# Kernel tuning notes

Measured on AMD Instinct MI355X. Metric: run time of the kernel, lower is better.

The kernel has to match this reference:

```python
import jax, jax.numpy as jnp
import numpy as np

N, E, F_IN, F_OUT, E_DIM = 8192, 65536, 256, 64, 32


def _xavier(k, shape, gain):
    fan_out, fan_in = shape
    bound = gain * jnp.sqrt(6.0 / (fan_in + fan_out))
    return jax.random.uniform(k, shape, jnp.float32, -bound, bound)


def setup_inputs() -> dict:
    key = jax.random.key(0)
    ks = jax.random.split(key, 10)
    gain = float(np.sqrt(2.0))  # calculate_gain('relu')
    return {
        "h_neigh": jax.random.normal(ks[0], (N, F_IN), jnp.float32),
        "h_self": jax.random.normal(ks[1], (N, F_IN), jnp.float32),
        "edge_features": jax.random.normal(ks[2], (E, E_DIM), jnp.float32),
        "W_preagg": _xavier(ks[3], (F_OUT, F_IN), gain),
        "W_self": _xavier(ks[4], (F_OUT, F_OUT), gain),
        "W_neigh": _xavier(ks[5], (F_OUT, F_OUT), gain),
        "W_edge": _xavier(ks[6], (F_OUT * F_OUT, E_DIM), gain),
        "b_edge": jnp.zeros((F_OUT * F_OUT,), jnp.float32),
        "src": jax.random.randint(ks[7], (E,), 0, N, jnp.int32),
        "dst": jax.random.randint(ks[8], (E,), 0, N, jnp.int32),
    }


def reference(h_neigh, h_self, edge_features, W_preagg, W_self, W_neigh, W_edge, b_edge, src, dst):
    relu = jax.nn.relu
    # fc_preagg (Linear no-bias + ReLU); dropout p=0 -> identity (eval mode)
    hn = relu(h_neigh @ W_preagg.T)   # [N, F_OUT]
    hs = relu(h_self @ W_preagg.T)    # [N, F_OUT]
    # edge_fc: Linear(edge_dim, F*F) + ReLU, viewed as [E, F, F]
    ew = relu(edge_features @ W_edge.T + b_edge).reshape(E, F_OUT, F_OUT)
    # DGL u_mul_e broadcast: m[e,i,j] = hn[src[e], j] * ew[e,i,j]
    # then mean over in-edges per dst node, then sum over dim i.
    # mean/sum commute with the i-sum, so fold i first: s[e,j] = sum_i ew[e,i,j]
    s = ew.sum(axis=1)                # [E, F_OUT]
    msg = hn[src] * s                 # [E, F_OUT]
    agg = jax.ops.segment_sum(msg, dst, num_segments=N)                      # [N, F_OUT]
    deg = jax.ops.segment_sum(jnp.ones((E,), jnp.float32), dst, num_segments=N)
    neigh = agg / jnp.maximum(deg, 1.0)[:, None]  # mean (0 for isolated nodes, as DGL)
    # fc_self / fc_neigh each include a ReLU, plus the outer ReLU
    z = relu(relu(hs @ W_self.T) + relu(neigh @ W_neigh.T))
    return z
```

## Files before the change

### kernel.cpp

```cpp
#include <hip/hip_runtime.h>
#include <hip/hip_bf16.h>

typedef __attribute__((ext_vector_type(8))) short bf16x8;
typedef __attribute__((ext_vector_type(8))) _Float16 f16x8;
typedef __attribute__((ext_vector_type(4))) float f32x4;

#define NNODES 8192
#define NEDGES 65536
#define FIN 256
#define FOUT 64
#define EDIM 32

#define WS_HN    0x000000u
#define WS_HS    0x200000u
#define WS_MSG   0x400000u
#define WS_DEG   0x1400000u
#define WS_OFF   0x1408000u
#define WS_RANK  0x1410000u
#define WS_PERM  0x1450000u
#define WS_GSRC  0x1490000u
#define WS_WEH   0x14D0000u
#define WS_WPH   0x1550000u
#define WS_WPL   0x1558000u
#define WS_WST   0x1560000u
#define WS_WNT   0x1564000u

__device__ __forceinline__ unsigned short f2bf(float f) {
    unsigned u = __builtin_bit_cast(unsigned, f);
    u = (u + 0x7fffu + ((u >> 16) & 1u)) >> 16;
    return (unsigned short)u;
}
__device__ __forceinline__ float bf2f(unsigned short h) {
    unsigned u = ((unsigned)h) << 16;
    return __builtin_bit_cast(float, u);
}
__device__ __forceinline__ void split8(float4 v0, float4 v1, bf16x8& hi, bf16x8& lo) {
    float x[8] = {v0.x, v0.y, v0.z, v0.w, v1.x, v1.y, v1.z, v1.w};
    #pragma unroll
    for (int j = 0; j < 8; ++j) {
        unsigned short h = f2bf(x[j]);
        hi[j] = (short)h;
        lo[j] = (short)f2bf(x[j] - bf2f(h));
    }
}
__device__ __forceinline__ f16x8 pack8h(float4 v0, float4 v1) {
    f16x8 r;
    r[0] = (_Float16)v0.x; r[1] = (_Float16)v0.y;
    r[2] = (_Float16)v0.z; r[3] = (_Float16)v0.w;
    r[4] = (_Float16)v1.x; r[5] = (_Float16)v1.y;
    r[6] = (_Float16)v1.z; r[7] = (_Float16)v1.w;
    return r;
}

__global__ __launch_bounds__(256) void prep_count_kernel(
    const float* __restrict__ W_edge,
    const float* __restrict__ W_preagg,
    const float* __restrict__ W_self,
    const float* __restrict__ W_neigh,
    const int* __restrict__ dst,
    _Float16* __restrict__ weh,
    unsigned short* __restrict__ wph,
    unsigned short* __restrict__ wpl,
    float* __restrict__ wsT,
    float* __restrict__ wnT,
    int* __restrict__ deg,
    int* __restrict__ rank) {
    int b = blockIdx.x, t = threadIdx.x;
    if (b < 512) {
        int i = b * 256 + t;
        if (i < FOUT * FOUT * EDIM)
            weh[i] = (_Float16)W_edge[i];
        if (i < FOUT * FIN) {
            float wv = W_preagg[i];
            unsigned short h = f2bf(wv);
            wph[i] = h;
            wpl[i] = f2bf(wv - bf2f(h));
        }
        if (i < FOUT * FOUT) {
            int o = i >> 6, k = i & 63;
            wsT[k * FOUT + o] = W_self[i];
            wnT[k * FOUT + o] = W_neigh[i];
        }
    } else {
        int e = (b - 512) * 256 + t;
        rank[e] = atomicAdd(deg + dst[e], 1);
    }
}

__global__ __launch_bounds__(256) void preagg_scan_kernel(
    const float* __restrict__ h_neigh,
    const float* __restrict__ h_self,
    const unsigned short* __restrict__ wph,
    const unsigned short* __restrict__ wpl,
    const int* __restrict__ deg,
    float* __restrict__ hn,
    float* __restrict__ hs,
    int* __restrict__ off) {
    __shared__ int wsum[4];
    int b = blockIdx.x, t = threadIdx.x;
    if (b == 256) {
        int lane = t & 63, w = t >> 6;
        int base = t * 32;
        int loc[32];
        int s = 0;
        #pragma unroll
        for (int i = 0; i < 32; ++i) { loc[i] = s; s += deg[base + i]; }
        int v = s;
        #pragma unroll
        for (int d = 1; d < 64; d <<= 1) {
            int u = __shfl_up(v, d);
            if (lane >= d) v += u;
        }
        if (lane == 63) wsum[w] = v;
        int threadExcl = v - s;
        __syncthreads();
        int wexcl = 0;
        for (int i = 0; i < w; ++i) wexcl += wsum[i];
        int tbase = wexcl + threadExcl;
        #pragma unroll
        for (int i = 0; i < 32; ++i) off[base + i] = tbase + loc[i];
        return;
    }
    int w = t >> 6, lane = t & 63;
    int rowm = lane & 15, kc = lane >> 4;
    int g0 = (b * 4 + w) * 16;
    const float* hsrc;
    float* outp;
    int r0;
    if (g0 < NNODES) { hsrc = h_neigh; outp = hn; r0 = g0; }
    else             { hsrc = h_self;  outp = hs; r0 = g0 - NNODES; }
    const float* arow = hsrc + (size_t)(r0 + rowm) * FIN;

    f32x4 acc[4];
    #pragma unroll
    for (int ot = 0; ot < 4; ++ot) acc[ot] = f32x4{0.f, 0.f, 0.f, 0.f};

    #pragma unroll 2
    for (int ks = 0; ks < 8; ++ks) {
        const float* p = arow + ks * 32 + kc * 8;
        float4 v0 = reinterpret_cast<const float4*>(p)[0];
        float4 v1 = reinterpret_cast<const float4*>(p)[1];
        bf16x8 ahi, alo;
        split8(v0, v1, ahi, alo);
        #pragma unroll
        for (int ot = 0; ot < 4; ++ot) {
            int woff = (ot * 16 + rowm) * FIN + ks * 32 + kc * 8;
            bf16x8 bh = *reinterpret_cast<const bf16x8*>(wph + woff);
            bf16x8 bl = *reinterpret_cast<const bf16x8*>(wpl + woff);
            acc[ot] = __builtin_amdgcn_mfma_f32_16x16x32_bf16(ahi, bh, acc[ot], 0, 0, 0);
            acc[ot] = __builtin_amdgcn_mfma_f32_16x16x32_bf16(alo, bh, acc[ot], 0, 0, 0);
            acc[ot] = __builtin_amdgcn_mfma_f32_16x16x32_bf16(ahi, bl, acc[ot], 0, 0, 0);
        }
    }
    #pragma unroll
    for (int ot = 0; ot < 4; ++ot)
        #pragma unroll
        for (int r = 0; r < 4; ++r)
            outp[(size_t)(r0 + kc * 4 + r) * FOUT + ot * 16 + rowm] =
                fmaxf(acc[ot][r], 0.f);
}

__global__ void fill_kernel(const int* __restrict__ src,
                            const int* __restrict__ dst,
                            const int* __restrict__ off,
                            const int* __restrict__ rank,
                            int* __restrict__ perm,
                            int* __restrict__ gsrc) {
    int e = blockIdx.x * 256 + threadIdx.x;
    int slot = off[dst[e]] + rank[e];
    perm[slot] = e;
    gsrc[slot] = src[e];
}

__global__ __launch_bounds__(256) void edge_kernel(
    const float* __restrict__ ef,
    const _Float16* __restrict__ weh,
    const float* __restrict__ b_edge,
    const float* __restrict__ hn,
    const int* __restrict__ perm,
    const int* __restrict__ gsrc,
    float* __restrict__ msg) {
    int t = threadIdx.x;
    int cw = t >> 6, lane = t & 63;
    int rowm = lane & 15, kc = lane >> 4, k0 = kc * 8;
    int e0 = blockIdx.x * 64;
    int colbase = cw * 16 + rowm;

    f16x8 a[4];
    #pragma unroll
    for (int tt = 0; tt < 4; ++tt) {
        int eidx = perm[e0 + tt * 16 + rowm];
        const float* p = ef + (size_t)eidx * EDIM + k0;
        float4 v0 = reinterpret_cast<const float4*>(p)[0];
        float4 v1 = reinterpret_cast<const float4*>(p)[1];
        a[tt] = pack8h(v0, v1);
    }

    f32x4 sacc[4];
    #pragma unroll
    for (int tt = 0; tt < 4; ++tt) sacc[tt] = f32x4{0.f, 0.f, 0.f, 0.f};
    const f32x4 z4 = {0.f, 0.f, 0.f, 0.f};

    const _Float16* wp = weh + ((size_t)colbase * 32 + kc * 8);
    const float* bp = b_edge + colbase;

    #pragma unroll 4
    for (int g = 0; g < 64; ++g) {
        f16x8 bh = *reinterpret_cast<const f16x8*>(wp);
        float bias = *bp;
        wp += 2048;
        bp += 64;
        f32x4 cin = {bias, bias, bias, bias};
        #pragma unroll
        for (int tt = 0; tt < 4; ++tt) {
            f32x4 d = __builtin_amdgcn_mfma_f32_16x16x32_f16(a[tt], bh, cin, 0, 0, 0);
            sacc[tt] += __builtin_elementwise_max(d, z4);
        }
    }

    #pragma unroll
    for (int tt = 0; tt < 4; ++tt) {
        #pragma unroll
        for (int r = 0; r < 4; ++r) {
            int slot = e0 + tt * 16 + kc * 4 + r;
            int se = gsrc[slot];
            float hv = hn[(size_t)se * FOUT + colbase];
            msg[(size_t)slot * FOUT + colbase] = sacc[tt][r] * hv;
        }
    }
}

__global__ __launch_bounds__(256) void final_kernel(
    const float* __restrict__ hs,
    const float* __restrict__ msg,
    const int* __restrict__ deg,
    const int* __restrict__ off,
    const float* __restrict__ wsT,
    const float* __restrict__ wnT,
    float* __restrict__ out) {
    __shared__ float sm[4][2][FOUT];
    int t = threadIdx.x, w = t >> 6, lane = t & 63;
    int n = blockIdx.x * 4 + w;
    int o0 = off[n], d = deg[n];
    const float* mp = msg + (size_t)o0 * FOUT + lane;
    float acc = 0.f;
    int i = 0;
    for (; i + 4 <= d; i += 4) {
        float m0 = mp[(size_t)(i + 0) * FOUT];
        float m1 = mp[(size_t)(i + 1) * FOUT];
        float m2 = mp[(size_t)(i + 2) * FOUT];
        float m3 = mp[(size_t)(i + 3) * FOUT];
        acc += (m0 + m1) + (m2 + m3);
    }
    for (; i < d; ++i) acc += mp[(size_t)i * FOUT];
    float neigh = acc / fmaxf((float)d, 1.f);
    sm[w][0][lane] = neigh;
    sm[w][1][lane] = hs[(size_t)n * FOUT + lane];
    __syncthreads();
    float a1 = 0.f, a2 = 0.f;
    #pragma unroll 8
    for (int k = 0; k < FOUT; ++k) {
        a1 = fmaf(sm[w][1][k], wsT[k * FOUT + lane], a1);
        a2 = fmaf(sm[w][0][k], wnT[k * FOUT + lane], a2);
    }
    out[(size_t)n * FOUT + lane] = fmaxf(fmaxf(a1, 0.f) + fmaxf(a2, 0.f), 0.f);
}

extern "C" void kernel_launch(void* const* d_in, const int* in_sizes, int n_in,
                              void* d_out, int out_size, void* d_ws, size_t ws_size,
                              hipStream_t stream) {
    const float* h_neigh  = (const float*)d_in[0];
    const float* h_self   = (const float*)d_in[1];
    const float* ef       = (const float*)d_in[2];
    const float* W_preagg = (const float*)d_in[3];
    const float* W_self   = (const float*)d_in[4];
    const float* W_neigh  = (const float*)d_in[5];
    const float* W_edge   = (const float*)d_in[6];
    const float* b_edge   = (const float*)d_in[7];
    const int*   src      = (const int*)d_in[8];
    const int*   dst      = (const int*)d_in[9];
    float* out = (float*)d_out;
    char* ws = (char*)d_ws;

    float* hn    = (float*)(ws + WS_HN);
    float* hs    = (float*)(ws + WS_HS);
    float* msg   = (float*)(ws + WS_MSG);
    int*   deg   = (int*)(ws + WS_DEG);
    int*   off   = (int*)(ws + WS_OFF);
    int*   rank  = (int*)(ws + WS_RANK);
    int*   perm  = (int*)(ws + WS_PERM);
    int*   gsrc  = (int*)(ws + WS_GSRC);
    _Float16* weh = (_Float16*)(ws + WS_WEH);
    unsigned short* wph = (unsigned short*)(ws + WS_WPH);
    unsigned short* wpl = (unsigned short*)(ws + WS_WPL);
    float* wsT   = (float*)(ws + WS_WST);
    float* wnT   = (float*)(ws + WS_WNT);

    hipMemsetAsync(ws + WS_DEG, 0, 0x8000, stream);

    prep_count_kernel<<<768, 256, 0, stream>>>(W_edge, W_preagg, W_self, W_neigh,
                                               dst, weh, wph, wpl, wsT, wnT,
                                               deg, rank);
    preagg_scan_kernel<<<257, 256, 0, stream>>>(h_neigh, h_self, wph, wpl, deg,
                                                hn, hs, off);
    fill_kernel<<<NEDGES / 256, 256, 0, stream>>>(src, dst, off, rank, perm, gsrc);
    edge_kernel<<<1024, 256, 0, stream>>>(ef, weh, b_edge, hn, perm, gsrc, msg);
    final_kernel<<<NNODES / 4, 256, 0, stream>>>(hs, msg, deg, off, wsT, wnT, out);
}
```

Before: 88.09 us.

## Use relu(x)=(x+|x|)/2 identity with folded weights; single-pass fp16 preagg GEMM

```diff
diff --git a/kernel.cpp b/kernel.cpp
--- a/kernel.cpp
+++ b/kernel.cpp
@@ -1,7 +1,6 @@
 #include <hip/hip_runtime.h>
 #include <hip/hip_bf16.h>
 
-typedef __attribute__((ext_vector_type(8))) short bf16x8;
 typedef __attribute__((ext_vector_type(8))) _Float16 f16x8;
 typedef __attribute__((ext_vector_type(4))) float f32x4;
 
@@ -20,29 +19,12 @@
 #define WS_PERM  0x1450000u
 #define WS_GSRC  0x1490000u
 #define WS_WEH   0x14D0000u
-#define WS_WPH   0x1550000u
-#define WS_WPL   0x1558000u
-#define WS_WST   0x1560000u
-#define WS_WNT   0x1564000u
-
-__device__ __forceinline__ unsigned short f2bf(float f) {
-    unsigned u = __builtin_bit_cast(unsigned, f);
-    u = (u + 0x7fffu + ((u >> 16) & 1u)) >> 16;
-    return (unsigned short)u;
-}
-__device__ __forceinline__ float bf2f(unsigned short h) {
-    unsigned u = ((unsigned)h) << 16;
-    return __builtin_bit_cast(float, u);
-}
-__device__ __forceinline__ void split8(float4 v0, float4 v1, bf16x8& hi, bf16x8& lo) {
-    float x[8] = {v0.x, v0.y, v0.z, v0.w, v1.x, v1.y, v1.z, v1.w};
-    #pragma unroll
-    for (int j = 0; j < 8; ++j) {
-        unsigned short h = f2bf(x[j]);
-        hi[j] = (short)h;
-        lo[j] = (short)f2bf(x[j] - bf2f(h));
-    }
-}
+#define WS_WPREH 0x1510000u
+#define WS_WFH   0x1518000u
+#define WS_BF    0x1519000u
+#define WS_WST   0x1520000u
+#define WS_WNT   0x1524000u
+
 __device__ __forceinline__ f16x8 pack8h(float4 v0, float4 v1) {
     f16x8 r;
     r[0] = (_Float16)v0.x; r[1] = (_Float16)v0.y;
@@ -57,10 +39,12 @@
     const float* __restrict__ W_preagg,
     const float* __restrict__ W_self,
     const float* __restrict__ W_neigh,
+    const float* __restrict__ b_edge,
     const int* __restrict__ dst,
     _Float16* __restrict__ weh,
-    unsigned short* __restrict__ wph,
-    unsigned short* __restrict__ wpl,
+    _Float16* __restrict__ wpreh,
+    _Float16* __restrict__ wfh,
+    float* __restrict__ bfold,
     float* __restrict__ wsT,
     float* __restrict__ wnT,
     int* __restrict__ deg,
@@ -70,28 +54,37 @@
         int i = b * 256 + t;
         if (i < FOUT * FOUT * EDIM)
             weh[i] = (_Float16)W_edge[i];
-        if (i < FOUT * FIN) {
-            float wv = W_preagg[i];
-            unsigned short h = f2bf(wv);
-            wph[i] = h;
-            wpl[i] = f2bf(wv - bf2f(h));
-        }
+        if (i < FOUT * FIN)
+            wpreh[i] = (_Float16)W_preagg[i];
         if (i < FOUT * FOUT) {
             int o = i >> 6, k = i & 63;
             wsT[k * FOUT + o] = W_self[i];
             wnT[k * FOUT + o] = W_neigh[i];
         }
-    } else {
+    } else if (b < 768) {
         int e = (b - 512) * 256 + t;
         rank[e] = atomicAdd(deg + dst[e], 1);
+    } else {
+        int idx = (b - 768) * 256 + t;
+        int j = idx >> 5, k = idx & 31;
+        float s = 0.f;
+        #pragma unroll 4
+        for (int i = 0; i < 64; ++i)
+            s += W_edge[(i * 64 + j) * 32 + k];
+        wfh[j * 32 + k] = (_Float16)s;
+        if (idx < 64) {
+            float sb = 0.f;
+            #pragma unroll 4
+            for (int i = 0; i < 64; ++i) sb += b_edge[i * 64 + idx];
+            bfold[idx] = sb;
+        }
     }
 }
 
 __global__ __launch_bounds__(256) void preagg_scan_kernel(
     const float* __restrict__ h_neigh,
     const float* __restrict__ h_self,
-    const unsigned short* __restrict__ wph,
-    const unsigned short* __restrict__ wpl,
+    const _Float16* __restrict__ wpreh,
     const int* __restrict__ deg,
     float* __restrict__ hn,
     float* __restrict__ hs,
@@ -140,16 +133,12 @@
         const float* p = arow + ks * 32 + kc * 8;
         float4 v0 = reinterpret_cast<const float4*>(p)[0];
         float4 v1 = reinterpret_cast<const float4*>(p)[1];
-        bf16x8 ahi, alo;
-        split8(v0, v1, ahi, alo);
+        f16x8 af = pack8h(v0, v1);
         #pragma unroll
         for (int ot = 0; ot < 4; ++ot) {
-            int woff = (ot * 16 + rowm) * FIN + ks * 32 + kc * 8;
-            bf16x8 bh = *reinterpret_cast<const bf16x8*>(wph + woff);
-            bf16x8 bl = *reinterpret_cast<const bf16x8*>(wpl + woff);
-            acc[ot] = __builtin_amdgcn_mfma_f32_16x16x32_bf16(ahi, bh, acc[ot], 0, 0, 0);
-            acc[ot] = __builtin_amdgcn_mfma_f32_16x16x32_bf16(alo, bh, acc[ot], 0, 0, 0);
-            acc[ot] = __builtin_amdgcn_mfma_f32_16x16x32_bf16(ahi, bl, acc[ot], 0, 0, 0);
+            f16x8 bh = *reinterpret_cast<const f16x8*>(
+                wpreh + ((ot * 16 + rowm) * FIN + ks * 32 + kc * 8));
+            acc[ot] = __builtin_amdgcn_mfma_f32_16x16x32_f16(af, bh, acc[ot], 0, 0, 0);
         }
     }
     #pragma unroll
@@ -176,6 +165,8 @@
     const float* __restrict__ ef,
     const _Float16* __restrict__ weh,
     const float* __restrict__ b_edge,
+    const _Float16* __restrict__ wfh,
+    const float* __restrict__ bfold,
     const float* __restrict__ hn,
     const int* __restrict__ perm,
     const int* __restrict__ gsrc,
@@ -196,36 +187,43 @@
         a[tt] = pack8h(v0, v1);
     }
 
-    f32x4 sacc[4];
-    #pragma unroll
-    for (int tt = 0; tt < 4; ++tt) sacc[tt] = f32x4{0.f, 0.f, 0.f, 0.f};
-    const f32x4 z4 = {0.f, 0.f, 0.f, 0.f};
-
-    const _Float16* wp = weh + ((size_t)colbase * 32 + kc * 8);
-    const float* bp = b_edge + colbase;
+    f16x8 wf = *reinterpret_cast<const f16x8*>(wfh + colbase * 32 + kc * 8);
+    float bf = bfold[colbase];
+
+    f32x4 sabs[4];
+    #pragma unroll
+    for (int tt = 0; tt < 4; ++tt) sabs[tt] = f32x4{0.f, 0.f, 0.f, 0.f};
+    const f32x4 zc = {0.f, 0.f, 0.f, 0.f};
+
+    unsigned wofs = (unsigned)colbase * 32 + (unsigned)kc * 8;
+    unsigned bofs = (unsigned)colbase;
 
     #pragma unroll 4
     for (int g = 0; g < 64; ++g) {
-        f16x8 bh = *reinterpret_cast<const f16x8*>(wp);
-        float bias = *bp;
-        wp += 2048;
-        bp += 64;
-        f32x4 cin = {bias, bias, bias, bias};
+        f16x8 bh = *reinterpret_cast<const f16x8*>(weh + wofs);
+        float bias = b_edge[bofs];
+        wofs += 2048;
+        bofs += 64;
         #pragma unroll
         for (int tt = 0; tt < 4; ++tt) {
-            f32x4 d = __builtin_amdgcn_mfma_f32_16x16x32_f16(a[tt], bh, cin, 0, 0, 0);
-            sacc[tt] += __builtin_elementwise_max(d, z4);
+            f32x4 d = __builtin_amdgcn_mfma_f32_16x16x32_f16(a[tt], bh, zc, 0, 0, 0);
+            sabs[tt][0] += __builtin_fabsf(d[0] + bias);
+            sabs[tt][1] += __builtin_fabsf(d[1] + bias);
+            sabs[tt][2] += __builtin_fabsf(d[2] + bias);
+            sabs[tt][3] += __builtin_fabsf(d[3] + bias);
         }
     }
 
     #pragma unroll
     for (int tt = 0; tt < 4; ++tt) {
+        f32x4 cin = {bf, bf, bf, bf};
+        f32x4 d2 = __builtin_amdgcn_mfma_f32_16x16x32_f16(a[tt], wf, cin, 0, 0, 0);
         #pragma unroll
         for (int r = 0; r < 4; ++r) {
             int slot = e0 + tt * 16 + kc * 4 + r;
             int se = gsrc[slot];
-            float hv = hn[(size_t)se * FOUT + colbase];
-            msg[(size_t)slot * FOUT + colbase] = sacc[tt][r] * hv;
+            float hv = 0.5f * hn[(size_t)se * FOUT + colbase];
+            msg[(size_t)slot * FOUT + colbase] = (d2[r] + sabs[tt][r]) * hv;
         }
     }
 }
@@ -290,20 +288,22 @@
     int*   rank  = (int*)(ws + WS_RANK);
     int*   perm  = (int*)(ws + WS_PERM);
     int*   gsrc  = (int*)(ws + WS_GSRC);
-    _Float16* weh = (_Float16*)(ws + WS_WEH);
-    unsigned short* wph = (unsigned short*)(ws + WS_WPH);
-    unsigned short* wpl = (unsigned short*)(ws + WS_WPL);
+    _Float16* weh   = (_Float16*)(ws + WS_WEH);
+    _Float16* wpreh = (_Float16*)(ws + WS_WPREH);
+    _Float16* wfh   = (_Float16*)(ws + WS_WFH);
+    float* bfold = (float*)(ws + WS_BF);
     float* wsT   = (float*)(ws + WS_WST);
     float* wnT   = (float*)(ws + WS_WNT);
 
     hipMemsetAsync(ws + WS_DEG, 0, 0x8000, stream);
 
-    prep_count_kernel<<<768, 256, 0, stream>>>(W_edge, W_preagg, W_self, W_neigh,
-                                               dst, weh, wph, wpl, wsT, wnT,
-                                               deg, rank);
-    preagg_scan_kernel<<<257, 256, 0, stream>>>(h_neigh, h_self, wph, wpl, deg,
+    prep_count_kernel<<<776, 256, 0, stream>>>(W_edge, W_preagg, W_self, W_neigh,
+                                               b_edge, dst, weh, wpreh, wfh, bfold,
+                                               wsT, wnT, deg, rank);
+    preagg_scan_kernel<<<257, 256, 0, stream>>>(h_neigh, h_self, wpreh, deg,
                                                 hn, hs, off);
     fill_kernel<<<NEDGES / 256, 256, 0, stream>>>(src, dst, off, rank, perm, gsrc);
-    edge_kernel<<<1024, 256, 0, stream>>>(ef, weh, b_edge, hn, perm, gsrc, msg);
+    edge_kernel<<<1024, 256, 0, stream>>>(ef, weh, b_edge, wfh, bfold, hn,
+                                          perm, gsrc, msg);
     final_kernel<<<NNODES / 4, 256, 0, stream>>>(hs, msg, deg, off, wsT, wnT, out);
 }
```

New measurement: 88.48 us. About the same (+0.4%).
